# Performance work log

Measured on AMD Instinct MI355X. Metric: run time of the kernel, lower is better.

## Reference

```python
import jax, jax.numpy as jnp
import numpy as np

B, N, D_MODEL, HEADS, DFF, M = 4, 4096, 1024, 16, 4096, 256
DH = D_MODEL // HEADS  # 64
EPS_K = 1e-4
LN_EPS = 1e-5


def setup_inputs() -> dict:
    key = jax.random.key(0)
    ks = jax.random.split(key, 12)
    s = 0.02
    return {
        "video": jax.random.normal(ks[0], (B, N, D_MODEL), jnp.float32),
        "Wq": jax.random.normal(ks[1], (D_MODEL, D_MODEL), jnp.float32) * s,
        "bq": jnp.zeros((D_MODEL,), jnp.float32),
        "Wk": jax.random.normal(ks[2], (D_MODEL, D_MODEL), jnp.float32) * s,
        "bk": jnp.zeros((D_MODEL,), jnp.float32),
        "Wv": jax.random.normal(ks[3], (D_MODEL, D_MODEL), jnp.float32) * s,
        "bv": jnp.zeros((D_MODEL,), jnp.float32),
        "Wo": jax.random.normal(ks[4], (D_MODEL, D_MODEL), jnp.float32) * s,
        "bo": jnp.zeros((D_MODEL,), jnp.float32),
        "proj": jax.random.normal(ks[5], (M, DH), jnp.float32),  # random-feature matrix (buffer)
        "W1": jax.random.normal(ks[6], (DFF, D_MODEL), jnp.float32) * s,
        "b1": jnp.zeros((DFF,), jnp.float32),
        "W2": jax.random.normal(ks[7], (D_MODEL, DFF), jnp.float32) * s,
        "b2": jnp.zeros((D_MODEL,), jnp.float32),
        "g2": jnp.ones((D_MODEL,), jnp.float32),
        "be2": jnp.zeros((D_MODEL,), jnp.float32),
        "g3": jnp.ones((D_MODEL,), jnp.float32),
        "be3": jnp.zeros((D_MODEL,), jnp.float32),
    }


def softmax_kernel(x, proj, is_query):
    # FAVOR+ positive softmax random features (Performer).
    # x: [b,h,n,dh], proj: [m,dh]
    norm = x.shape[-1] ** -0.25  # data normalizer 1/d^{1/4}
    ratio = proj.shape[0] ** -0.5
    xp = jnp.einsum("bhnd,md->bhnm", x * norm, proj)
    diag = jnp.sum(jnp.square(x), axis=-1, keepdims=True) * 0.5 * (norm * norm)
    if is_query:
        stab = jnp.max(xp, axis=-1, keepdims=True)
    else:
        stab = jnp.max(xp, axis=(-1, -2), keepdims=True)
    return ratio * (jnp.exp(xp - diag - stab) + EPS_K)


def layer_norm(x, g, b):
    mu = jnp.mean(x, axis=-1, keepdims=True)
    var = jnp.mean(jnp.square(x - mu), axis=-1, keepdims=True)
    return (x - mu) * jax.lax.rsqrt(var + LN_EPS) * g + b


def reference(video, Wq, bq, Wk, bk, Wv, bv, Wo, bo, proj,
              W1, b1, W2, b2, g2, be2, g3, be3):
    b, n, d = video.shape
    split = lambda t: t.reshape(b, n, HEADS, DH).transpose(0, 2, 1, 3)  # [b,h,n,dh]
    q = split(video @ Wq.T + bq)
    k = split(video @ Wk.T + bk)
    v = split(video @ Wv.T + bv)

    qp = softmax_kernel(q, proj, is_query=True)   # [b,h,n,m]
    kp = softmax_kernel(k, proj, is_query=False)  # [b,h,n,m]

    # Non-causal linear attention: O(n*m*dh) instead of O(n^2)
    k_sum = jnp.sum(kp, axis=2)                              # [b,h,m]
    denom = jnp.einsum("bhnm,bhm->bhn", qp, k_sum)           # [b,h,n]
    ctx = jnp.einsum("bhnm,bhnd->bhmd", kp, v)               # [b,h,m,dh]
    out = jnp.einsum("bhnm,bhmd->bhnd", qp, ctx) / denom[..., None]

    attn = out.transpose(0, 2, 1, 3).reshape(b, n, d) @ Wo.T + bo
    x = layer_norm(video + attn, g2, be2)  # dropout is identity in eval
    ff = jax.nn.relu(x @ W1.T + b1) @ W2.T + b2
    return layer_norm(x + ff, g3, be3)
```

## Files before the change

### kernel.cpp

```cpp
#include <hip/hip_runtime.h>
#include <hip/hip_bf16.h>

#define N_TOK   4096
#define DMODEL  1024
#define NHEADS  16
#define DH      64
#define MFEAT   256
#define DFF     4096
#define BATCH   4
#define ROWS    (BATCH * N_TOK)

#define NORMF      0.35355339059327373f
#define HALF_NORM2 0.0625f
#define RATIO      0.0625f
#define EPSK       1e-4f
#define LNEPS      1e-5f

typedef unsigned short ushort_t;
using bfrag = __attribute__((ext_vector_type(8))) short;
using facc  = __attribute__((ext_vector_type(4))) float;
using ush8  = __attribute__((ext_vector_type(8))) unsigned short;

__device__ __forceinline__ float b2f(ushort_t u) {
    return __bfloat162float(__builtin_bit_cast(__hip_bfloat16, u));
}
__device__ __forceinline__ ushort_t f2b(float f) {
    return __builtin_bit_cast(ushort_t, __float2bfloat16(f));
}
__device__ __forceinline__ void stC(float* p, float v) { *p = v; }
__device__ __forceinline__ void stC(ushort_t* p, float v) { *p = f2b(v); }

__device__ __forceinline__ unsigned fkey(float f) {
    unsigned u = __float_as_uint(f);
    return (u & 0x80000000u) ? ~u : (u | 0x80000000u);
}
__device__ __forceinline__ float fdec(unsigned k) {
    return (k & 0x80000000u) ? __uint_as_float(k ^ 0x80000000u) : __uint_as_float(~k);
}

__global__ __launch_bounds__(256) void cvt_bf16(const float* __restrict__ s,
                                                ushort_t* __restrict__ d, int n4) {
    int i = blockIdx.x * 256 + threadIdx.x;
    if (i >= n4) return;
    float4 v = ((const float4*)s)[i];
    ((ushort4*)d)[i] = make_ushort4(f2b(v.x), f2b(v.y), f2b(v.z), f2b(v.w));
}

template <int FJ, typename OT>
__global__ __launch_bounds__(256) void gemm_mfma(
    const ushort_t* __restrict__ A, const ushort_t* __restrict__ W,
    const float* __restrict__ bias, OT* __restrict__ C,
    int Nout, int K, int relu)
{
    constexpr int BN = FJ * 32;
    __shared__ short As[128][40];
    __shared__ short Ws[BN][40];
    const int t = threadIdx.x;
    const int m0 = blockIdx.y * 128, n0 = blockIdx.x * BN;
    const int lane = t & 63, wave = t >> 6;
    const int wr = (wave >> 1) * 64, wc = (wave & 1) * (FJ * 16);
    const int lm = lane & 15, kq = (lane >> 4) * 8;
    facc acc[4][FJ];
#pragma unroll
    for (int i = 0; i < 4; ++i)
#pragma unroll
        for (int j = 0; j < FJ; ++j) acc[i][j] = (facc){0.f, 0.f, 0.f, 0.f};

    for (int k0 = 0; k0 < K; k0 += 32) {
#pragma unroll
        for (int it = 0; it < 2; ++it) {
            int ch = t + it * 256;
            int row = ch >> 2, c8 = (ch & 3) * 8;
            *(uint4*)&As[row][c8] = *(const uint4*)(A + (size_t)(m0 + row) * K + k0 + c8);
        }
#pragma unroll
        for (int it = 0; it < BN / 64; ++it) {
            int ch = t + it * 256;
            int row = ch >> 2, c8 = (ch & 3) * 8;
            *(uint4*)&Ws[row][c8] = *(const uint4*)(W + (size_t)(n0 + row) * K + k0 + c8);
        }
        __syncthreads();
        bfrag af[4], bf[FJ];
#pragma unroll
        for (int i = 0; i < 4; ++i) af[i] = *(bfrag*)&As[wr + i * 16 + lm][kq];
#pragma unroll
        for (int j = 0; j < FJ; ++j) bf[j] = *(bfrag*)&Ws[wc + j * 16 + lm][kq];
#pragma unroll
        for (int i = 0; i < 4; ++i)
#pragma unroll
            for (int j = 0; j < FJ; ++j)
                acc[i][j] = __builtin_amdgcn_mfma_f32_16x16x32_bf16(af[i], bf[j], acc[i][j], 0, 0, 0);
        __syncthreads();
    }
    const int rq = (lane >> 4) * 4;
#pragma unroll
    for (int i = 0; i < 4; ++i)
#pragma unroll
        for (int j = 0; j < FJ; ++j) {
            int col = n0 + wc + j * 16 + lm;
            float bc = bias[col];
#pragma unroll
            for (int r = 0; r < 4; ++r) {
                int row = m0 + wr + i * 16 + rq + r;
                float v = acc[i][j][r] + bc;
                if (relu) v = fmaxf(v, 0.f);
                stC(C + (size_t)row * Nout + col, v);
            }
        }
}

__global__ __launch_bounds__(256) void vt_kernel(
    const ushort_t* __restrict__ V, ushort_t* __restrict__ VT)
{
    __shared__ ushort_t tile[64][68];
    const int t = threadIdx.x;
    const int n0 = blockIdx.x * 64, h = blockIdx.y;
#pragma unroll
    for (int i = 0; i < 4; ++i) {
        int idx = t + i * 256;
        int nl = idx >> 4, d4 = (idx & 15) * 4;
        ushort4 v = *(const ushort4*)(V + (size_t)(n0 + nl) * DMODEL + h * DH + d4);
        tile[nl][d4 + 0] = v.x; tile[nl][d4 + 1] = v.y;
        tile[nl][d4 + 2] = v.z; tile[nl][d4 + 3] = v.w;
    }
    __syncthreads();
#pragma unroll
    for (int i = 0; i < 4; ++i) {
        int idx = t + i * 256;
        int d = idx >> 4, n4 = (idx & 15) * 4;
        ushort4 o = make_ushort4(tile[n4][d], tile[n4 + 1][d], tile[n4 + 2][d], tile[n4 + 3][d]);
        *(ushort4*)(VT + (size_t)h * DH * N_TOK + (size_t)d * N_TOK + n0 + n4) = o;
    }
}

__global__ __launch_bounds__(256) void diagk_kernel(
    const ushort_t* __restrict__ Kb, float* __restrict__ diagK)
{
    const int lane = threadIdx.x & 63, wave = threadIdx.x >> 6;
    const int n = blockIdx.x * 4 + wave;
    const ushort_t* kr = Kb + (size_t)n * DMODEL + lane * 16;
    ush8 a = *(const ush8*)kr;
    ush8 b = *(const ush8*)(kr + 8);
    float s = 0.f;
#pragma unroll
    for (int e = 0; e < 8; ++e) { float x = b2f(a[e]); s += x * x; }
#pragma unroll
    for (int e = 0; e < 8; ++e) { float x = b2f(b[e]); s += x * x; }
    s += __shfl_xor(s, 1);
    s += __shfl_xor(s, 2);
    if ((lane & 3) == 0) diagK[(size_t)(lane >> 2) * N_TOK + n] = s;
}

__global__ __launch_bounds__(256) void xk_kernel(
    const ushort_t* __restrict__ projBF,
    const ushort_t* __restrict__ Kb,
    const float* __restrict__ diagK,
    unsigned* __restrict__ kmax16,
    ushort_t* __restrict__ KP,
    int mode)
{
    __shared__ short As[128][40];
    __shared__ short Ws[128][40];
    const int t = threadIdx.x;
    const int m0 = blockIdx.x * 128, n0 = blockIdx.y * 128, h = blockIdx.z;
    const ushort_t* Kh = Kb + h * DH;
    const int lane = t & 63, wave = t >> 6;
    const int wr = (wave >> 1) * 64, wc = (wave & 1) * 64;
    const int lm = lane & 15, kq = (lane >> 4) * 8;
    facc acc[4][4];
#pragma unroll
    for (int i = 0; i < 4; ++i)
#pragma unroll
        for (int j = 0; j < 4; ++j) acc[i][j] = (facc){0.f, 0.f, 0.f, 0.f};

    for (int k0 = 0; k0 < DH; k0 += 32) {
#pragma unroll
        for (int it = 0; it < 2; ++it) {
            int ch = t + it * 256;
            int row = ch >> 2, c8 = (ch & 3) * 8;
            *(uint4*)&As[row][c8] = *(const uint4*)(projBF + (size_t)(m0 + row) * DH + k0 + c8);
            *(uint4*)&Ws[row][c8] = *(const uint4*)(Kh + (size_t)(n0 + row) * DMODEL + k0 + c8);
        }
        __syncthreads();
        bfrag af[4], bf[4];
#pragma unroll
        for (int i = 0; i < 4; ++i) af[i] = *(bfrag*)&As[wr + i * 16 + lm][kq];
#pragma unroll
        for (int j = 0; j < 4; ++j) bf[j] = *(bfrag*)&Ws[wc + j * 16 + lm][kq];
#pragma unroll
        for (int i = 0; i < 4; ++i)
#pragma unroll
            for (int j = 0; j < 4; ++j)
                acc[i][j] = __builtin_amdgcn_mfma_f32_16x16x32_bf16(af[i], bf[j], acc[i][j], 0, 0, 0);
        __syncthreads();
    }
    const int rq = (lane >> 4) * 4;
    if (mode == 0) {
        float mx = -1e30f;
#pragma unroll
        for (int i = 0; i < 4; ++i)
#pragma unroll
            for (int j = 0; j < 4; ++j)
#pragma unroll
                for (int r = 0; r < 4; ++r) mx = fmaxf(mx, acc[i][j][r]);
        mx *= NORMF;
#pragma unroll
        for (int o = 32; o >= 1; o >>= 1) mx = fmaxf(mx, __shfl_xor(mx, o));
        if (lane == 0) atomicMax(kmax16 + h, fkey(mx));
    } else {
        const float stab = fdec(kmax16[h]);
        ushort_t* kb = KP + (size_t)h * MFEAT * N_TOK;
#pragma unroll
        for (int j = 0; j < 4; ++j) {
            int n = n0 + wc + j * 16 + lm;
            float dg = HALF_NORM2 * diagK[(size_t)h * N_TOK + n] + stab;
#pragma unroll
            for (int i = 0; i < 4; ++i)
#pragma unroll
                for (int r = 0; r < 4; ++r) {
                    int m = m0 + wr + i * 16 + rq + r;
                    float x = NORMF * acc[i][j][r];
                    kb[(size_t)m * N_TOK + n] = f2b(RATIO * (expf(x - dg) + EPSK));
                }
        }
    }
}

__global__ __launch_bounds__(256) void ksum_kernel(
    const ushort_t* __restrict__ KP, float* __restrict__ ksum)
{
    const int lane = threadIdx.x & 63, wave = threadIdx.x >> 6;
    const int row = blockIdx.x * 4 + wave;
    const ushort_t* kr = KP + (size_t)row * N_TOK;
    float s = 0.f;
#pragma unroll
    for (int it = 0; it < 8; ++it) {
        ush8 v = *(const ush8*)(kr + it * 512 + lane * 8);
#pragma unroll
        for (int e = 0; e < 8; ++e) s += b2f(v[e]);
    }
#pragma unroll
    for (int o = 32; o >= 1; o >>= 1) s += __shfl_xor(s, o);
    if (lane == 0) ksum[row] = s;
}

__global__ __launch_bounds__(256) void ctx_mfma(
    const ushort_t* __restrict__ KP, const ushort_t* __restrict__ VT,
    float* __restrict__ ctx)
{
    __shared__ short As[128][40];
    __shared__ short Vs[64][40];
    const int t = threadIdx.x;
    const int z = blockIdx.x, mh = blockIdx.y, h = blockIdx.z;
    const ushort_t* A = KP + (size_t)h * MFEAT * N_TOK + (size_t)mh * 128 * N_TOK;
    const ushort_t* W = VT + (size_t)h * DH * N_TOK;
    const int lane = t & 63, wave = t >> 6;
    const int wr = (wave >> 1) * 64, wc = (wave & 1) * 32;
    const int lm = lane & 15, kq = (lane >> 4) * 8;
    facc acc[4][2];
#pragma unroll
    for (int i = 0; i < 4; ++i)
#pragma unroll
        for (int j = 0; j < 2; ++j) acc[i][j] = (facc){0.f, 0.f, 0.f, 0.f};

    const int kbeg = z * 512, kend = kbeg + 512;
    for (int k0 = kbeg; k0 < kend; k0 += 32) {
#pragma unroll
        for (int it = 0; it < 2; ++it) {
            int ch = t + it * 256;
            int row = ch >> 2, c8 = (ch & 3) * 8;
            *(uint4*)&As[row][c8] = *(const uint4*)(A + (size_t)row * N_TOK + k0 + c8);
        }
        {
            int row = t >> 2, c8 = (t & 3) * 8;
            *(uint4*)&Vs[row][c8] = *(const uint4*)(W + (size_t)row * N_TOK + k0 + c8);
        }
        __syncthreads();
        bfrag af[4], bf[2];
#pragma unroll
        for (int i = 0; i < 4; ++i) af[i] = *(bfrag*)&As[wr + i * 16 + lm][kq];
#pragma unroll
        for (int j = 0; j < 2; ++j) bf[j] = *(bfrag*)&Vs[wc + j * 16 + lm][kq];
#pragma unroll
        for (int i = 0; i < 4; ++i)
#pragma unroll
            for (int j = 0; j < 2; ++j)
                acc[i][j] = __builtin_amdgcn_mfma_f32_16x16x32_bf16(af[i], bf[j], acc[i][j], 0, 0, 0);
        __syncthreads();
    }
    const int rq = (lane >> 4) * 4;
    float* cb = ctx + (size_t)h * MFEAT * DH + (size_t)mh * 128 * DH;
#pragma unroll
    for (int i = 0; i < 4; ++i)
#pragma unroll
        for (int j = 0; j < 2; ++j)
#pragma unroll
            for (int r = 0; r < 4; ++r) {
                int m = wr + i * 16 + rq + r;
                int d = wc + j * 16 + lm;
                atomicAdd(cb + (size_t)m * DH + d, acc[i][j][r]);
            }
}

__global__ __launch_bounds__(256) void ctx_transpose(
    const float* __restrict__ ctx, ushort_t* __restrict__ ctxT)
{
    __shared__ float tile[64][65];
    const int bh = blockIdx.x, t = threadIdx.x;
    const float* cb = ctx + (size_t)bh * MFEAT * DH;
    ushort_t* ob = ctxT + (size_t)bh * DH * MFEAT;
    for (int mb = 0; mb < 4; ++mb) {
#pragma unroll
        for (int i = 0; i < 16; ++i) {
            int idx = t + i * 256;
            tile[idx >> 6][idx & 63] = cb[(size_t)(mb * 64 + (idx >> 6)) * DH + (idx & 63)];
        }
        __syncthreads();
#pragma unroll
        for (int i = 0; i < 16; ++i) {
            int idx = t + i * 256;
            ob[(size_t)(idx >> 6) * MFEAT + mb * 64 + (idx & 63)] = f2b(tile[idx & 63][idx >> 6]);
        }
        __syncthreads();
    }
}

__global__ __launch_bounds__(256) void xp_gemm(
    const float* __restrict__ Q, const ushort_t* __restrict__ projBF,
    ushort_t* __restrict__ XP)
{
    __shared__ short As[128][40];
    __shared__ short Ws[128][40];
    const int t = threadIdx.x;
    const int m0 = blockIdx.x * 128, n0v = blockIdx.y * 128, h = blockIdx.z;
    const float* Qb = Q + h * DH;
    const int lane = t & 63, wave = t >> 6;
    const int wr = (wave >> 1) * 64, wc = (wave & 1) * 64;
    const int lm = lane & 15, kq = (lane >> 4) * 8;
    facc acc[4][4];
#pragma unroll
    for (int i = 0; i < 4; ++i)
#pragma unroll
        for (int j = 0; j < 4; ++j) acc[i][j] = (facc){0.f, 0.f, 0.f, 0.f};

    for (int k0 = 0; k0 < 64; k0 += 32) {
#pragma unroll
        for (int it = 0; it < 4; ++it) {
            int ch = t + it * 256;
            int row = ch >> 3, c4 = (ch & 7) * 4;
            float4 v = *(const float4*)(Qb + (size_t)(n0v + row) * DMODEL + k0 + c4);
            As[row][c4 + 0] = (short)f2b(v.x);
            As[row][c4 + 1] = (short)f2b(v.y);
            As[row][c4 + 2] = (short)f2b(v.z);
            As[row][c4 + 3] = (short)f2b(v.w);
        }
#pragma unroll
        for (int it = 0; it < 2; ++it) {
            int ch = t + it * 256;
            int row = ch >> 2, c8 = (ch & 3) * 8;
            *(uint4*)&Ws[row][c8] = *(const uint4*)(projBF + (size_t)(m0 + row) * DH + k0 + c8);
        }
        __syncthreads();
        bfrag af[4], bf[4];
#pragma unroll
        for (int i = 0; i < 4; ++i) af[i] = *(bfrag*)&As[wr + i * 16 + lm][kq];
#pragma unroll
        for (int j = 0; j < 4; ++j) bf[j] = *(bfrag*)&Ws[wc + j * 16 + lm][kq];
#pragma unroll
        for (int i = 0; i < 4; ++i)
#pragma unroll
            for (int j = 0; j < 4; ++j)
                acc[i][j] = __builtin_amdgcn_mfma_f32_16x16x32_bf16(af[i], bf[j], acc[i][j], 0, 0, 0);
        __syncthreads();
    }
    const int rq = (lane >> 4) * 4;
    ushort_t* xb = XP + (size_t)h * N_TOK * MFEAT;
#pragma unroll
    for (int i = 0; i < 4; ++i)
#pragma unroll
        for (int j = 0; j < 4; ++j) {
            int col = m0 + wc + j * 16 + lm;
#pragma unroll
            for (int r = 0; r < 4; ++r) {
                int row = n0v + wr + i * 16 + rq + r;
                xb[(size_t)row * MFEAT + col] = f2b(NORMF * acc[i][j][r]);
            }
        }
}

__global__ __launch_bounds__(256) void qp_kernel(
    ushort_t* __restrict__ XP, const float* __restrict__ Q,
    const float* __restrict__ ksum, float* __restrict__ denom)
{
    const int lane = threadIdx.x & 63, wave = threadIdx.x >> 6;
    const int row0 = (blockIdx.x * 4 + wave) * 8;
    for (int rr = 0; rr < 8; ++rr) {
        const int row = row0 + rr;
        const int h = row >> 12, n = row & 4095;
        ushort_t* xr = XP + (size_t)row * MFEAT + lane * 4;
        ushort4 xv = *(ushort4*)xr;
        float x0 = b2f(xv.x), x1 = b2f(xv.y), x2 = b2f(xv.z), x3 = b2f(xv.w);
        float qv = Q[(size_t)n * DMODEL + h * DH + lane];
        float ss = qv * qv;
#pragma unroll
        for (int o = 32; o >= 1; o >>= 1) ss += __shfl_xor(ss, o);
        float mx = fmaxf(fmaxf(x0, x1), fmaxf(x2, x3));
#pragma unroll
        for (int o = 32; o >= 1; o >>= 1) mx = fmaxf(mx, __shfl_xor(mx, o));
        const float sh = HALF_NORM2 * ss + mx;
        float p0 = RATIO * (expf(x0 - sh) + EPSK);
        float p1 = RATIO * (expf(x1 - sh) + EPSK);
        float p2 = RATIO * (expf(x2 - sh) + EPSK);
        float p3 = RATIO * (expf(x3 - sh) + EPSK);
        ushort4 pv = make_ushort4(f2b(p0), f2b(p1), f2b(p2), f2b(p3));
        *(ushort4*)xr = pv;
        float4 ks4 = *(const float4*)(ksum + h * MFEAT + lane * 4);
        float dn = b2f(pv.x) * ks4.x + b2f(pv.y) * ks4.y + b2f(pv.z) * ks4.z + b2f(pv.w) * ks4.w;
#pragma unroll
        for (int o = 32; o >= 1; o >>= 1) dn += __shfl_xor(dn, o);
        if (lane == 0) denom[row] = dn;
    }
}

__global__ __launch_bounds__(256) void out_gemm(
    const ushort_t* __restrict__ XP, const ushort_t* __restrict__ ctxT,
    const float* __restrict__ denom, ushort_t* __restrict__ OUT)
{
    __shared__ short As[128][40];
    __shared__ short Ws[64][40];
    const int t = threadIdx.x;
    const int n0 = blockIdx.x * 128, h = blockIdx.y;
    const ushort_t* A = XP + (size_t)h * N_TOK * MFEAT;
    const ushort_t* W = ctxT + (size_t)h * DH * MFEAT;
    const float* dnb = denom + (size_t)h * N_TOK;
    ushort_t* ob = OUT + h * DH;
    const int lane = t & 63, wave = t >> 6;
    const int wr = (wave >> 1) * 64, wc = (wave & 1) * 32;
    const int lm = lane & 15, kq = (lane >> 4) * 8;
    facc acc[4][2];
#pragma unroll
    for (int i = 0; i < 4; ++i)
#pragma unroll
        for (int j = 0; j < 2; ++j) acc[i][j] = (facc){0.f, 0.f, 0.f, 0.f};

    for (int k0 = 0; k0 < MFEAT; k0 += 32) {
#pragma unroll
        for (int it = 0; it < 2; ++it) {
            int ch = t + it * 256;
            int row = ch >> 2, c8 = (ch & 3) * 8;
            *(uint4*)&As[row][c8] = *(const uint4*)(A + (size_t)(n0 + row) * MFEAT + k0 + c8);
        }
        {
            int row = t >> 2, c8 = (t & 3) * 8;
            *(uint4*)&Ws[row][c8] = *(const uint4*)(W + (size_t)row * MFEAT + k0 + c8);
        }
        __syncthreads();
        bfrag af[4], bf[2];
#pragma unroll
        for (int i = 0; i < 4; ++i) af[i] = *(bfrag*)&As[wr + i * 16 + lm][kq];
#pragma unroll
        for (int j = 0; j < 2; ++j) bf[j] = *(bfrag*)&Ws[wc + j * 16 + lm][kq];
#pragma unroll
        for (int i = 0; i < 4; ++i)
#pragma unroll
            for (int j = 0; j < 2; ++j)
                acc[i][j] = __builtin_amdgcn_mfma_f32_16x16x32_bf16(af[i], bf[j], acc[i][j], 0, 0, 0);
        __syncthreads();
    }
    const int rq = (lane >> 4) * 4;
#pragma unroll
    for (int i = 0; i < 4; ++i)
#pragma unroll
        for (int r = 0; r < 4; ++r) {
            int row = n0 + wr + i * 16 + rq + r;
            float inv = 1.f / dnb[row];
#pragma unroll
            for (int j = 0; j < 2; ++j) {
                int col = wc + j * 16 + lm;
                ob[(size_t)row * DMODEL + col] = f2b(acc[i][j][r] * inv);
            }
        }
}

__global__ __launch_bounds__(256) void ln_kernel(
    const float* __restrict__ A, const void* __restrict__ Badd, int badd_bf16,
    const float* __restrict__ g, const float* __restrict__ bb,
    float* __restrict__ out, ushort_t* __restrict__ out_bf)
{
    __shared__ float red[256];
    const int row = blockIdx.x, t = threadIdx.x;
    const float* a = A + (size_t)row * DMODEL;
    float v[4];
    float s = 0.f;
#pragma unroll
    for (int i = 0; i < 4; ++i) {
        int col = t + i * 256;
        float add = badd_bf16 ? b2f(((const ushort_t*)Badd)[(size_t)row * DMODEL + col])
                              : ((const float*)Badd)[(size_t)row * DMODEL + col];
        v[i] = a[col] + add;
        s += v[i];
    }
    red[t] = s;
    __syncthreads();
    for (int st = 128; st > 0; st >>= 1) { if (t < st) red[t] += red[t + st]; __syncthreads(); }
    float mu = red[0] * (1.f / DMODEL);
    __syncthreads();
    float sq = 0.f;
#pragma unroll
    for (int i = 0; i < 4; ++i) { float dlt = v[i] - mu; sq += dlt * dlt; }
    red[t] = sq;
    __syncthreads();
    for (int st = 128; st > 0; st >>= 1) { if (t < st) red[t] += red[t + st]; __syncthreads(); }
    float rstd = rsqrtf(red[0] * (1.f / DMODEL) + LNEPS);
    float* o = out + (size_t)row * DMODEL;
#pragma unroll
    for (int i = 0; i < 4; ++i) {
        int col = t + i * 256;
        float val = (v[i] - mu) * rstd * g[col] + bb[col];
        o[col] = val;
        if (out_bf) out_bf[(size_t)row * DMODEL + col] = f2b(val);
    }
}

extern "C" void kernel_launch(void* const* d_in, const int* in_sizes, int n_in,
                              void* d_out, int out_size, void* d_ws, size_t ws_size,
                              hipStream_t stream)
{
    const float* video = (const float*)d_in[0];
    const float* Wq = (const float*)d_in[1];
    const float* bq = (const float*)d_in[2];
    const float* Wk = (const float*)d_in[3];
    const float* bk = (const float*)d_in[4];
    const float* Wv = (const float*)d_in[5];
    const float* bv = (const float*)d_in[6];
    const float* Wo = (const float*)d_in[7];
    const float* bo = (const float*)d_in[8];
    const float* proj = (const float*)d_in[9];
    const float* W1 = (const float*)d_in[10];
    const float* b1 = (const float*)d_in[11];
    const float* W2 = (const float*)d_in[12];
    const float* b2 = (const float*)d_in[13];
    const float* g2 = (const float*)d_in[14];
    const float* be2 = (const float*)d_in[15];
    const float* g3 = (const float*)d_in[16];
    const float* be3 = (const float*)d_in[17];

    char* ws = (char*)d_ws;
    const size_t MB = 1048576ull;
    ushort_t* videoBF = (ushort_t*)(ws + 0);
    ushort_t* Kb   = (ushort_t*)(ws + 32 * MB);
    ushort_t* XBFb = (ushort_t*)(ws + 32 * MB);
    ushort_t* Vb   = (ushort_t*)(ws + 40 * MB);
    ushort_t* Fb   = (ushort_t*)(ws + 40 * MB);
    ushort_t* VTb  = (ushort_t*)(ws + 48 * MB);
    ushort_t* Yb   = (ushort_t*)(ws + 48 * MB);
    ushort_t* KP   = (ushort_t*)(ws + 56 * MB);
    ushort_t* Hb   = (ushort_t*)(ws + 56 * MB);
    float*    ctxb = (float*)(ws + 93847552ull);
    ushort_t* ctxTb = (ushort_t*)(ws + 93847552ull + MB);
    char* smalls = ws + 91 * MB + 393216ull;
    float*    diagK  = (float*)(smalls);
    float*    ksum   = (float*)(smalls + 262144);
    float*    denomB = (float*)(smalls + 278528);
    unsigned* kmax16 = (unsigned*)(smalls + 540672);
    ushort_t* projBF = (ushort_t*)(smalls + 541184);
    ushort_t* OUTb = (ushort_t*)(ws + 92 * MB);
    ushort_t* WqBF = (ushort_t*)(ws + 100 * MB);
    ushort_t* WkBF = (ushort_t*)(ws + 102 * MB);
    ushort_t* WvBF = (ushort_t*)(ws + 104 * MB);
    ushort_t* WoBF = (ushort_t*)(ws + 106 * MB);
    ushort_t* W1BF = (ushort_t*)(ws + 108 * MB);
    ushort_t* W2BF = (ushort_t*)(ws + 116 * MB);
    float* Qbuf = (float*)d_out;

    dim3 blk(256);

    cvt_bf16<<<dim3(ROWS * DMODEL / 1024), blk, 0, stream>>>(video, videoBF, ROWS * DMODEL / 4);
    cvt_bf16<<<dim3(DMODEL * DMODEL / 1024), blk, 0, stream>>>(Wq, WqBF, DMODEL * DMODEL / 4);
    cvt_bf16<<<dim3(DMODEL * DMODEL / 1024), blk, 0, stream>>>(Wk, WkBF, DMODEL * DMODEL / 4);
    cvt_bf16<<<dim3(DMODEL * DMODEL / 1024), blk, 0, stream>>>(Wv, WvBF, DMODEL * DMODEL / 4);
    cvt_bf16<<<dim3(DMODEL * DMODEL / 1024), blk, 0, stream>>>(Wo, WoBF, DMODEL * DMODEL / 4);
    cvt_bf16<<<dim3(DFF * DMODEL / 1024), blk, 0, stream>>>(W1, W1BF, DFF * DMODEL / 4);
    cvt_bf16<<<dim3(DFF * DMODEL / 1024), blk, 0, stream>>>(W2, W2BF, DFF * DMODEL / 4);
    cvt_bf16<<<dim3(16), blk, 0, stream>>>(proj, projBF, MFEAT * DH / 4);

    gemm_mfma<4, float><<<dim3(8, ROWS / 128), blk, 0, stream>>>(
        videoBF, WqBF, bq, Qbuf, DMODEL, DMODEL, 0);

    dim3 gP(8, 32);

    for (int b = 0; b < BATCH; ++b) {
        const size_t roff = (size_t)b * N_TOK;
        const ushort_t* vbf = videoBF + roff * DMODEL;
        float* Qb = Qbuf + roff * DMODEL;

        gemm_mfma<4, ushort_t><<<gP, blk, 0, stream>>>(vbf, WkBF, bk, Kb, DMODEL, DMODEL, 0);
        gemm_mfma<4, ushort_t><<<gP, blk, 0, stream>>>(vbf, WvBF, bv, Vb, DMODEL, DMODEL, 0);
        vt_kernel<<<dim3(64, 16), blk, 0, stream>>>(Vb, VTb);
        diagk_kernel<<<dim3(1024), blk, 0, stream>>>(Kb, diagK);

        hipMemsetAsync(ctxb, 0, MB, stream);
        hipMemsetAsync(kmax16, 0, 64, stream);

        xk_kernel<<<dim3(2, 32, 16), blk, 0, stream>>>(projBF, Kb, diagK, kmax16, KP, 0);
        xk_kernel<<<dim3(2, 32, 16), blk, 0, stream>>>(projBF, Kb, diagK, kmax16, KP, 1);
        ksum_kernel<<<dim3(1024), blk, 0, stream>>>(KP, ksum);
        ctx_mfma<<<dim3(8, 2, 16), blk, 0, stream>>>(KP, VTb, ctxb);
        ctx_transpose<<<dim3(16), blk, 0, stream>>>(ctxb, ctxTb);

        xp_gemm<<<dim3(2, 32, 16), blk, 0, stream>>>(Qb, projBF, KP);
        qp_kernel<<<dim3(2048), blk, 0, stream>>>(KP, Qb, ksum, denomB);
        out_gemm<<<dim3(32, 16), blk, 0, stream>>>(KP, ctxTb, denomB, OUTb);

        gemm_mfma<4, ushort_t><<<gP, blk, 0, stream>>>(OUTb, WoBF, bo, Yb, DMODEL, DMODEL, 0);
        ln_kernel<<<dim3(N_TOK), blk, 0, stream>>>(
            video + roff * DMODEL, Yb, 1, g2, be2, Qb, XBFb);
        gemm_mfma<4, ushort_t><<<dim3(32, 32), blk, 0, stream>>>(
            XBFb, W1BF, b1, Hb, DFF, DMODEL, 1);
        gemm_mfma<2, ushort_t><<<dim3(16, 32), blk, 0, stream>>>(
            Hb, W2BF, b2, Fb, DMODEL, DFF, 0);
        ln_kernel<<<dim3(N_TOK), blk, 0, stream>>>(
            Qb, Fb, 1, g3, be3, Qb, nullptr);
    }
}
```

Before: 1.836 ms.

## Use direct global-to-LDS loads in all MFMA GEMMs and swizzle GEMM workgroup order

Replaces register-staged global-to-shared copies with buffer/global_load_lds direct-to-LDS transfers in the projection, feature, context and output GEMMs. To fit the contiguous per-lane write pattern of that instruction, the LDS tiles drop their padding (stride 40 to 32). The main GEMM also remaps workgroup IDs so consecutive blocks are spread across 8 XCD-like groups, aiming for better L2 reuse. The unpadded LDS layout may cause bank conflicts on the fragment reads, and the remap assumes the block count divides evenly by 8.

Result: faster. 1.760 ms (-4.1%).

```diff
diff --git a/kernel.cpp b/kernel.cpp
--- a/kernel.cpp
+++ b/kernel.cpp
@@ -30,6 +30,12 @@
 __device__ __forceinline__ void stC(float* p, float v) { *p = v; }
 __device__ __forceinline__ void stC(ushort_t* p, float v) { *p = f2b(v); }
 
+__device__ __forceinline__ void gload_lds16(const void* g, void* l) {
+    __builtin_amdgcn_global_load_lds(
+        (const __attribute__((address_space(1))) unsigned int*)g,
+        (__attribute__((address_space(3))) unsigned int*)l, 16, 0, 0);
+}
+
 __device__ __forceinline__ unsigned fkey(float f) {
     unsigned u = __float_as_uint(f);
     return (u & 0x80000000u) ? ~u : (u | 0x80000000u);
@@ -53,10 +59,14 @@
     int Nout, int K, int relu)
 {
     constexpr int BN = FJ * 32;
-    __shared__ short As[128][40];
-    __shared__ short Ws[BN][40];
+    __shared__ short As[128 * 32];
+    __shared__ short Ws[BN * 32];
     const int t = threadIdx.x;
-    const int m0 = blockIdx.y * 128, n0 = blockIdx.x * BN;
+    const unsigned nwg = gridDim.x * gridDim.y;
+    const unsigned flat = blockIdx.y * gridDim.x + blockIdx.x;
+    const unsigned cpx = nwg >> 3;
+    const unsigned wg = (flat & 7) * cpx + (flat >> 3);
+    const int m0 = (int)(wg / gridDim.x) * 128, n0 = (int)(wg % gridDim.x) * BN;
     const int lane = t & 63, wave = t >> 6;
     const int wr = (wave >> 1) * 64, wc = (wave & 1) * (FJ * 16);
     const int lm = lane & 15, kq = (lane >> 4) * 8;
@@ -71,20 +81,20 @@
         for (int it = 0; it < 2; ++it) {
             int ch = t + it * 256;
             int row = ch >> 2, c8 = (ch & 3) * 8;
-            *(uint4*)&As[row][c8] = *(const uint4*)(A + (size_t)(m0 + row) * K + k0 + c8);
+            gload_lds16(A + (size_t)(m0 + row) * K + k0 + c8, &As[ch * 8]);
         }
 #pragma unroll
         for (int it = 0; it < BN / 64; ++it) {
             int ch = t + it * 256;
             int row = ch >> 2, c8 = (ch & 3) * 8;
-            *(uint4*)&Ws[row][c8] = *(const uint4*)(W + (size_t)(n0 + row) * K + k0 + c8);
+            gload_lds16(W + (size_t)(n0 + row) * K + k0 + c8, &Ws[ch * 8]);
         }
         __syncthreads();
         bfrag af[4], bf[FJ];
 #pragma unroll
-        for (int i = 0; i < 4; ++i) af[i] = *(bfrag*)&As[wr + i * 16 + lm][kq];
-#pragma unroll
-        for (int j = 0; j < FJ; ++j) bf[j] = *(bfrag*)&Ws[wc + j * 16 + lm][kq];
+        for (int i = 0; i < 4; ++i) af[i] = *(bfrag*)&As[(wr + i * 16 + lm) * 32 + kq];
+#pragma unroll
+        for (int j = 0; j < FJ; ++j) bf[j] = *(bfrag*)&Ws[(wc + j * 16 + lm) * 32 + kq];
 #pragma unroll
         for (int i = 0; i < 4; ++i)
 #pragma unroll
@@ -159,8 +169,8 @@
     ushort_t* __restrict__ KP,
     int mode)
 {
-    __shared__ short As[128][40];
-    __shared__ short Ws[128][40];
+    __shared__ short As[128 * 32];
+    __shared__ short Ws[128 * 32];
     const int t = threadIdx.x;
     const int m0 = blockIdx.x * 128, n0 = blockIdx.y * 128, h = blockIdx.z;
     const ushort_t* Kh = Kb + h * DH;
@@ -178,15 +188,15 @@
         for (int it = 0; it < 2; ++it) {
             int ch = t + it * 256;
             int row = ch >> 2, c8 = (ch & 3) * 8;
-            *(uint4*)&As[row][c8] = *(const uint4*)(projBF + (size_t)(m0 + row) * DH + k0 + c8);
-            *(uint4*)&Ws[row][c8] = *(const uint4*)(Kh + (size_t)(n0 + row) * DMODEL + k0 + c8);
+            gload_lds16(projBF + (size_t)(m0 + row) * DH + k0 + c8, &As[ch * 8]);
+            gload_lds16(Kh + (size_t)(n0 + row) * DMODEL + k0 + c8, &Ws[ch * 8]);
         }
         __syncthreads();
         bfrag af[4], bf[4];
 #pragma unroll
-        for (int i = 0; i < 4; ++i) af[i] = *(bfrag*)&As[wr + i * 16 + lm][kq];
-#pragma unroll
-        for (int j = 0; j < 4; ++j) bf[j] = *(bfrag*)&Ws[wc + j * 16 + lm][kq];
+        for (int i = 0; i < 4; ++i) af[i] = *(bfrag*)&As[(wr + i * 16 + lm) * 32 + kq];
+#pragma unroll
+        for (int j = 0; j < 4; ++j) bf[j] = *(bfrag*)&Ws[(wc + j * 16 + lm) * 32 + kq];
 #pragma unroll
         for (int i = 0; i < 4; ++i)
 #pragma unroll
@@ -248,8 +258,8 @@
     const ushort_t* __restrict__ KP, const ushort_t* __restrict__ VT,
     float* __restrict__ ctx)
 {
-    __shared__ short As[128][40];
-    __shared__ short Vs[64][40];
+    __shared__ short As[128 * 32];
+    __shared__ short Vs[64 * 32];
     const int t = threadIdx.x;
     const int z = blockIdx.x, mh = blockIdx.y, h = blockIdx.z;
     const ushort_t* A = KP + (size_t)h * MFEAT * N_TOK + (size_t)mh * 128 * N_TOK;
@@ -269,18 +279,18 @@
         for (int it = 0; it < 2; ++it) {
             int ch = t + it * 256;
             int row = ch >> 2, c8 = (ch & 3) * 8;
-            *(uint4*)&As[row][c8] = *(const uint4*)(A + (size_t)row * N_TOK + k0 + c8);
+            gload_lds16(A + (size_t)row * N_TOK + k0 + c8, &As[ch * 8]);
         }
         {
             int row = t >> 2, c8 = (t & 3) * 8;
-            *(uint4*)&Vs[row][c8] = *(const uint4*)(W + (size_t)row * N_TOK + k0 + c8);
+            gload_lds16(W + (size_t)row * N_TOK + k0 + c8, &Vs[t * 8]);
         }
         __syncthreads();
         bfrag af[4], bf[2];
 #pragma unroll
-        for (int i = 0; i < 4; ++i) af[i] = *(bfrag*)&As[wr + i * 16 + lm][kq];
-#pragma unroll
-        for (int j = 0; j < 2; ++j) bf[j] = *(bfrag*)&Vs[wc + j * 16 + lm][kq];
+        for (int i = 0; i < 4; ++i) af[i] = *(bfrag*)&As[(wr + i * 16 + lm) * 32 + kq];
+#pragma unroll
+        for (int j = 0; j < 2; ++j) bf[j] = *(bfrag*)&Vs[(wc + j * 16 + lm) * 32 + kq];
 #pragma unroll
         for (int i = 0; i < 4; ++i)
 #pragma unroll
@@ -426,8 +436,8 @@
     const ushort_t* __restrict__ XP, const ushort_t* __restrict__ ctxT,
     const float* __restrict__ denom, ushort_t* __restrict__ OUT)
 {
-    __shared__ short As[128][40];
-    __shared__ short Ws[64][40];
+    __shared__ short As[128 * 32];
+    __shared__ short Ws[64 * 32];
     const int t = threadIdx.x;
     const int n0 = blockIdx.x * 128, h = blockIdx.y;
     const ushort_t* A = XP + (size_t)h * N_TOK * MFEAT;
@@ -448,18 +458,18 @@
         for (int it = 0; it < 2; ++it) {
             int ch = t + it * 256;
             int row = ch >> 2, c8 = (ch & 3) * 8;
-            *(uint4*)&As[row][c8] = *(const uint4*)(A + (size_t)(n0 + row) * MFEAT + k0 + c8);
+            gload_lds16(A + (size_t)(n0 + row) * MFEAT + k0 + c8, &As[ch * 8]);
         }
         {
             int row = t >> 2, c8 = (t & 3) * 8;
-            *(uint4*)&Ws[row][c8] = *(const uint4*)(W + (size_t)row * MFEAT + k0 + c8);
+            gload_lds16(W + (size_t)row * MFEAT + k0 + c8, &Ws[t * 8]);
         }
         __syncthreads();
         bfrag af[4], bf[2];
 #pragma unroll
-        for (int i = 0; i < 4; ++i) af[i] = *(bfrag*)&As[wr + i * 16 + lm][kq];
-#pragma unroll
-        for (int j = 0; j < 2; ++j) bf[j] = *(bfrag*)&Ws[wc + j * 16 + lm][kq];
+        for (int i = 0; i < 4; ++i) af[i] = *(bfrag*)&As[(wr + i * 16 + lm) * 32 + kq];
+#pragma unroll
+        for (int j = 0; j < 2; ++j) bf[j] = *(bfrag*)&Ws[(wc + j * 16 + lm) * 32 + kq];
 #pragma unroll
         for (int i = 0; i < 4; ++i)
 #pragma unroll
```
